# Optimization experiments

Measured on AMD Instinct MI355X. Metric: run time of the kernel, lower is better.

Reference implementation:

```python
import jax, jax.numpy as jnp
import numpy as np

B, N, D, H, O = 4096, 128, 64, 256, 128  # batch, memory_size, memory_dim, controller_dim, output_size


def setup_inputs() -> dict:
    key = jax.random.key(0)
    ks = jax.random.split(key, 20)
    s = 0.05
    inp = {
        "x": jax.random.normal(ks[0], (B, O), jnp.float32),
        "memory": jax.random.normal(ks[1], (B, N, D), jnp.float32),
        "h": jax.random.normal(ks[2], (B, H), jnp.float32),
        "c": jax.random.normal(ks[3], (B, H), jnp.float32),
        # LSTMCell params (torch layout: gates ordered i, f, g, o; input = x||read_vec of width O+D)
        "W_ih": jax.random.normal(ks[4], (4 * H, O + D), jnp.float32) * s,
        "W_hh": jax.random.normal(ks[5], (4 * H, H), jnp.float32) * s,
        "b_ih": jax.random.normal(ks[6], (4 * H,), jnp.float32) * s,
        "b_hh": jax.random.normal(ks[7], (4 * H,), jnp.float32) * s,
        "W_read": jax.random.normal(ks[8], (N, H), jnp.float32) * s,
        "b_read": jax.random.normal(ks[9], (N,), jnp.float32) * s,
        "W_write": jax.random.normal(ks[10], (N, H), jnp.float32) * s,
        "b_write": jax.random.normal(ks[11], (N,), jnp.float32) * s,
        "W_erase": jax.random.normal(ks[12], (D, H), jnp.float32) * s,
        "b_erase": jax.random.normal(ks[13], (D,), jnp.float32) * s,
        "W_add": jax.random.normal(ks[14], (D, H), jnp.float32) * s,
        "b_add": jax.random.normal(ks[15], (D,), jnp.float32) * s,
        "W_out": jax.random.normal(ks[16], (O, H + D), jnp.float32) * s,
        "b_out": jax.random.normal(ks[17], (O,), jnp.float32) * s,
    }
    return inp


def reference(x, memory, h, c, W_ih, W_hh, b_ih, b_hh, W_read, b_read,
              W_write, b_write, W_erase, b_erase, W_add, b_add, W_out, b_out):
    # read: softmax attention over memory rows, addressed by previous hidden state
    read_w = jax.nn.softmax(h @ W_read.T + b_read, axis=-1)          # [B, N]
    read_vec = jnp.einsum("bn,bnd->bd", read_w, memory)               # [B, D]

    # LSTMCell step (torch gate order: i, f, g, o)
    ctrl_in = jnp.concatenate([x, read_vec], axis=-1)                 # [B, O+D]
    gates = ctrl_in @ W_ih.T + b_ih + h @ W_hh.T + b_hh               # [B, 4H]
    i, f, g, o = jnp.split(gates, 4, axis=-1)
    i, f, o = jax.nn.sigmoid(i), jax.nn.sigmoid(f), jax.nn.sigmoid(o)
    g = jnp.tanh(g)
    c_new = f * c + i * g
    h_new = o * jnp.tanh(c_new)

    # write: outer-product erase/add update
    write_w = jax.nn.softmax(h_new @ W_write.T + b_write, axis=-1)    # [B, N]
    erase = jax.nn.sigmoid(h_new @ W_erase.T + b_erase)               # [B, D]
    add = jnp.tanh(h_new @ W_add.T + b_add)                           # [B, D]
    ww = write_w[:, :, None]                                          # [B, N, 1]
    mem_new = memory * (1.0 - ww * erase[:, None, :]) + ww * add[:, None, :]

    out = jnp.concatenate([h_new, read_vec], axis=-1) @ W_out.T + b_out  # [B, O]
    return (out, mem_new, h_new, c_new)
```

## Files before the change

kernel.cpp:

```cpp
#include <hip/hip_runtime.h>
#include <math.h>


typedef __attribute__((ext_vector_type(8))) short bf16x8;
typedef __attribute__((ext_vector_type(4))) float f32x4;
typedef __attribute__((ext_vector_type(4))) unsigned short us4;

#define MFMA16(a, b, c) __builtin_amdgcn_mfma_f32_16x16x32_bf16(a, b, c, 0, 0, 0)
#define GLL16(gp, lp) __builtin_amdgcn_global_load_lds( \
    (const __attribute__((address_space(1))) void*)(gp), \
    (__attribute__((address_space(3))) void*)(lp), 16, 0, 0)
#define SW(row, s) ((s) ^ ((row) & 3))

__device__ __forceinline__ float sigf(float v) { return 1.f / (1.f + __expf(-v)); }

__device__ __forceinline__ unsigned short f2bf(float f) {
    unsigned u = __builtin_bit_cast(unsigned, f);
    u = (u + 0x7FFFu + ((u >> 16) & 1u)) >> 16;
    return (unsigned short)u;
}

__device__ __forceinline__ int swA(int r, int c) {
    return r * 320 + (c & ~31) + ((((c >> 3) & 3) ^ (r & 3)) << 3) + (c & 7);
}

__global__ __launch_bounds__(256) void kA_scores(
    const float* __restrict__ h, const float* __restrict__ Wr,
    const float* __restrict__ br, float* __restrict__ read_w)
{
    __shared__ unsigned short As[16 * 32];
    __shared__ unsigned short Bs[128 * 32];
    __shared__ float sc[16][128];

    int t = threadIdx.x;
    int wid = t >> 6, lane = t & 63;
    int cl = lane & 15, ks = lane >> 4;
    int b0 = blockIdx.x * 16;

    int aOff = cl * 32 + SW(cl, ks) * 8;
    int bOff[4];
#pragma unroll
    for (int f = 0; f < 4; ++f) {
        int br_ = (wid * 4 + f) * 16 + cl;
        bOff[f] = br_ * 32 + SW(br_, ks) * 8;
    }
    f32x4 acc[4] = {};
    for (int kc = 0; kc < 8; ++kc) {
        __syncthreads();
        {
            int row = t >> 4, k0 = (t & 15) * 2;
            float2 hv = *(const float2*)(h + (size_t)(b0 + row) * 256 + kc * 32 + k0);
            unsigned pk = (unsigned)f2bf(hv.x) | ((unsigned)f2bf(hv.y) << 16);
            *(unsigned*)(As + row * 32 + SW(row, k0 >> 3) * 8 + (k0 & 7)) = pk;
        }
        {
            int row = t >> 1, k0 = (t & 1) * 16;
            const float4* wp = (const float4*)(Wr + (size_t)row * 256 + kc * 32 + k0);
            float4 w0 = wp[0], w1 = wp[1], w2 = wp[2], w3 = wp[3];
            us4 p0 = { f2bf(w0.x), f2bf(w0.y), f2bf(w0.z), f2bf(w0.w) };
            us4 p1 = { f2bf(w1.x), f2bf(w1.y), f2bf(w1.z), f2bf(w1.w) };
            us4 p2 = { f2bf(w2.x), f2bf(w2.y), f2bf(w2.z), f2bf(w2.w) };
            us4 p3 = { f2bf(w3.x), f2bf(w3.y), f2bf(w3.z), f2bf(w3.w) };
            int g0 = k0 >> 3;
            unsigned short* basep = Bs + row * 32;
            *(us4*)(basep + SW(row, g0) * 8)         = p0;
            *(us4*)(basep + SW(row, g0) * 8 + 4)     = p1;
            *(us4*)(basep + SW(row, g0 + 1) * 8)     = p2;
            *(us4*)(basep + SW(row, g0 + 1) * 8 + 4) = p3;
        }
        __syncthreads();
        if (wid < 2) {
            bf16x8 a = *(const bf16x8*)(As + aOff);
#pragma unroll
            for (int f = 0; f < 4; ++f)
                acc[f] = MFMA16(a, *(const bf16x8*)(Bs + bOff[f]), acc[f]);
        }
    }
    if (wid < 2) {
#pragma unroll
        for (int f = 0; f < 4; ++f)
#pragma unroll
            for (int r = 0; r < 4; ++r)
                sc[ks * 4 + r][(wid * 4 + f) * 16 + cl] = acc[f][r];
    }
    __syncthreads();
    {
        int row = t >> 4, l = t & 15;
        float v[8];
#pragma unroll
        for (int j = 0; j < 8; ++j) v[j] = sc[row][l + 16 * j] + br[l + 16 * j];
        float m = v[0];
#pragma unroll
        for (int j = 1; j < 8; ++j) m = fmaxf(m, v[j]);
#pragma unroll
        for (int mk = 8; mk >= 1; mk >>= 1) m = fmaxf(m, __shfl_xor(m, mk));
        float s = 0.f;
#pragma unroll
        for (int j = 0; j < 8; ++j) { v[j] = __expf(v[j] - m); s += v[j]; }
#pragma unroll
        for (int mk = 8; mk >= 1; mk >>= 1) s += __shfl_xor(s, mk);
        float inv = 1.f / s;
#pragma unroll
        for (int j = 0; j < 8; ++j)
            read_w[(size_t)(b0 + row) * 128 + l + 16 * j] = v[j] * inv;
    }
}

__global__ __launch_bounds__(256) void k2_stream_pack(
    const float* __restrict__ mem, const float* __restrict__ read_w,
    const float* __restrict__ x, const float* __restrict__ h,
    const float* __restrict__ Wih, const float* __restrict__ Whh,
    const float* __restrict__ bih, const float* __restrict__ bhh,
    const float* __restrict__ Ww, const float* __restrict__ We,
    const float* __restrict__ Wa, const float* __restrict__ bw,
    const float* __restrict__ be, const float* __restrict__ ba,
    const float* __restrict__ Wo,
    unsigned short* __restrict__ Wg, unsigned short* __restrict__ Wh_b,
    unsigned short* __restrict__ Wo_b, float* __restrict__ bsum,
    float* __restrict__ bh_b, unsigned short* __restrict__ Ag,
    float* __restrict__ rvf)
{
    __shared__ float part[16][68];
    int t = threadIdx.x;
    int b = blockIdx.x;
    unsigned idx = b * 256 + t;

    if (idx < 458752) {
        int r = idx / 448, cc = idx - r * 448;
        float v = (cc < 192) ? Wih[(size_t)r * 192 + cc] : Whh[(size_t)r * 256 + (cc - 192)];
        Wg[idx] = f2bf(v);
    }
    if (idx < 65536) {
        int r = idx >> 8, cc = idx & 255;
        float v = (r < 128) ? Ww[(size_t)r * 256 + cc]
                : (r < 192) ? We[(size_t)(r - 128) * 256 + cc]
                            : Wa[(size_t)(r - 192) * 256 + cc];
        Wh_b[idx] = f2bf(v);
    }
    if (idx < 40960) Wo_b[idx] = f2bf(Wo[idx]);
    if (idx < 1024)  bsum[idx] = bih[idx] + bhh[idx];
    if (idx < 256)
        bh_b[idx] = (idx < 128) ? bw[idx] : (idx < 192 ? be[idx - 128] : ba[idx - 192]);

    if (t < 96) {
        int j = t;
        float4 v = (j < 32) ? ((const float4*)(x + (size_t)b * 128))[j]
                            : ((const float4*)(h + (size_t)b * 256))[j - 32];
        us4 o = { f2bf(v.x), f2bf(v.y), f2bf(v.z), f2bf(v.w) };
        int col = (j < 32) ? j * 4 : 192 + (j - 32) * 4;
        *(us4*)(Ag + (size_t)b * 448 + col) = o;
    }

    int np = t >> 4, d4 = t & 15;
    const float4* m4 = (const float4*)(mem + (size_t)b * 8192);
    float4 acc = make_float4(0.f, 0.f, 0.f, 0.f);
#pragma unroll
    for (int j = 0; j < 8; ++j) {
        int n = np + 16 * j;
        float w = read_w[(size_t)b * 128 + n];
        float4 mv = m4[t + 256 * j];
        acc.x += w * mv.x; acc.y += w * mv.y; acc.z += w * mv.z; acc.w += w * mv.w;
    }
    part[np][d4 * 4 + 0] = acc.x; part[np][d4 * 4 + 1] = acc.y;
    part[np][d4 * 4 + 2] = acc.z; part[np][d4 * 4 + 3] = acc.w;
    __syncthreads();
    if (t < 64) {
        float s = 0.f;
#pragma unroll
        for (int q = 0; q < 16; ++q) s += part[q][t];
        Ag[(size_t)b * 448 + 128 + t] = f2bf(s);
        rvf[(size_t)b * 64 + t] = s;
    }
}

__global__ __launch_bounds__(256) void kB_gates(
    const unsigned short* __restrict__ Ag, const unsigned short* __restrict__ Wg,
    const float* __restrict__ bsum, const float* __restrict__ c,
    float* __restrict__ h_new, float* __restrict__ c_new)
{
    __shared__ unsigned short As[32 * 32];
    __shared__ unsigned short Bs[256 * 32];
    int t = threadIdx.x;
    int wid = t >> 6, lane = t & 63;
    int cl = lane & 15, ks = lane >> 4;
    int b0 = blockIdx.x * 32;
    int u0 = blockIdx.y * 64;

    int arow = (t >> 2) & 31;
    const unsigned short* aSrc = Ag + (size_t)(b0 + arow) * 448 + SW(arow, t & 3) * 8;
    unsigned short* aDst = As + wid * 512;
    const unsigned short* bSrc[4];
    unsigned short* bDst[4];
#pragma unroll
    for (int j = 0; j < 4; ++j) {
        int rl = (j * 256 + t) >> 2;
        int g = rl >> 6, u = rl & 63;
        bSrc[j] = Wg + (size_t)(g * 256 + u0 + u) * 448 + SW(rl, t & 3) * 8;
        bDst[j] = Bs + (j * 256 + wid * 64) * 8;
    }

    int aOff[2];
#pragma unroll
    for (int rf = 0; rf < 2; ++rf) {
        int mr = rf * 16 + cl;
        aOff[rf] = mr * 32 + SW(mr, ks) * 8;
    }
    int bOff[4];
#pragma unroll
    for (int g = 0; g < 4; ++g) {
        int br_ = g * 64 + wid * 16 + cl;
        bOff[g] = br_ * 32 + SW(br_, ks) * 8;
    }

    f32x4 acc[2][4] = {};
    for (int kc = 0; kc < 14; ++kc) {
        __syncthreads();
        if (wid < 2) GLL16(aSrc, aDst);
        GLL16(bSrc[0], bDst[0]); GLL16(bSrc[1], bDst[1]);
        GLL16(bSrc[2], bDst[2]); GLL16(bSrc[3], bDst[3]);
        aSrc += 32;
#pragma unroll
        for (int j = 0; j < 4; ++j) bSrc[j] += 32;
        __syncthreads();
        bf16x8 a[2], b[4];
#pragma unroll
        for (int rf = 0; rf < 2; ++rf) a[rf] = *(const bf16x8*)(As + aOff[rf]);
#pragma unroll
        for (int g = 0; g < 4; ++g) b[g] = *(const bf16x8*)(Bs + bOff[g]);
#pragma unroll
        for (int rf = 0; rf < 2; ++rf)
#pragma unroll
            for (int g = 0; g < 4; ++g)
                acc[rf][g] = MFMA16(a[rf], b[g], acc[rf][g]);
    }

    int unit = u0 + wid * 16 + cl;
    float bi = bsum[unit], bf_ = bsum[256 + unit];
    float bg = bsum[512 + unit], bo_ = bsum[768 + unit];
#pragma unroll
    for (int rf = 0; rf < 2; ++rf) {
#pragma unroll
        for (int r = 0; r < 4; ++r) {
            int row = b0 + rf * 16 + ks * 4 + r;
            float iv = sigf(acc[rf][0][r] + bi);
            float fv = sigf(acc[rf][1][r] + bf_);
            float gv = tanhf(acc[rf][2][r] + bg);
            float ov = sigf(acc[rf][3][r] + bo_);
            float cv = fv * c[(size_t)row * 256 + unit] + iv * gv;
            float hv = ov * tanhf(cv);
            c_new[(size_t)row * 256 + unit] = cv;
            h_new[(size_t)row * 256 + unit] = hv;
        }
    }
}

__global__ __launch_bounds__(256) void kC5(
    const float* __restrict__ h_new, const float* __restrict__ rvf,
    const unsigned short* __restrict__ Wh_b, const unsigned short* __restrict__ Wo_b,
    const float* __restrict__ bh_b, const float* __restrict__ bo,
    const float* __restrict__ mem, float* __restrict__ outp,
    float* __restrict__ mem_new)
{
    __shared__ unsigned short As[4 * 320];
    __shared__ unsigned short Bh[256 * 32];
    __shared__ unsigned short Bo[128 * 32];
    __shared__ float sc[4][384];
    __shared__ float wL[4][128];
    __shared__ __align__(16) float eL[4][64];
    __shared__ __align__(16) float aL[4][64];

    int t = threadIdx.x;
    int wid = t >> 6, lane = t & 63;
    int cl = lane & 15, ks = lane >> 4;
    int b0 = blockIdx.x * 4;

    for (int i = t; i < 4 * 320; i += 256) {
        int row = i / 320, col = i - row * 320;
        float v = (col < 256) ? h_new[(size_t)(b0 + row) * 256 + col]
                              : rvf[(size_t)(b0 + row) * 64 + (col - 256)];
        As[swA(row, col)] = f2bf(v);
    }

    const unsigned short* bhSrc[4];
    unsigned short* bhDst[4];
#pragma unroll
    for (int j = 0; j < 4; ++j) {
        int rl = (j * 256 + t) >> 2;
        bhSrc[j] = Wh_b + (size_t)rl * 256 + SW(rl, t & 3) * 8;
        bhDst[j] = Bh + (j * 256 + wid * 64) * 8;
    }
    const unsigned short* boSrc[2];
    unsigned short* boDst[2];
#pragma unroll
    for (int j = 0; j < 2; ++j) {
        int rj = j * 64 + (t >> 2);
        boSrc[j] = Wo_b + (size_t)rj * 320 + SW(rj, t & 3) * 8;
        boDst[j] = Bo + j * 2048 + wid * 512;
    }

    int bOffH[4], bOffO[2];
#pragma unroll
    for (int j = 0; j < 4; ++j) { int br_ = (wid + 4 * j) * 16 + cl; bOffH[j] = br_ * 32 + SW(br_, ks) * 8; }
#pragma unroll
    for (int j = 0; j < 2; ++j) { int br_ = (wid + 4 * j) * 16 + cl; bOffO[j] = br_ * 32 + SW(br_, ks) * 8; }

    f32x4 accH[4] = {};
    f32x4 accO[2] = {};
    for (int kc = 0; kc < 10; ++kc) {
        __syncthreads();
        if (kc < 8) {
            GLL16(bhSrc[0], bhDst[0]); GLL16(bhSrc[1], bhDst[1]);
            GLL16(bhSrc[2], bhDst[2]); GLL16(bhSrc[3], bhDst[3]);
#pragma unroll
            for (int j = 0; j < 4; ++j) bhSrc[j] += 32;
        }
        GLL16(boSrc[0], boDst[0]); GLL16(boSrc[1], boDst[1]);
#pragma unroll
        for (int j = 0; j < 2; ++j) boSrc[j] += 32;
        __syncthreads();
        bf16x8 a = *(const bf16x8*)(As + swA(cl & 3, kc * 32 + ks * 8));
        if (kc < 8) {
#pragma unroll
            for (int j = 0; j < 4; ++j)
                accH[j] = MFMA16(a, *(const bf16x8*)(Bh + bOffH[j]), accH[j]);
        }
#pragma unroll
        for (int j = 0; j < 2; ++j)
            accO[j] = MFMA16(a, *(const bf16x8*)(Bo + bOffO[j]), accO[j]);
    }

    if (ks == 0) {
#pragma unroll
        for (int j = 0; j < 4; ++j) {
            int col = (wid + 4 * j) * 16 + cl;
            float bb = bh_b[col];
#pragma unroll
            for (int r = 0; r < 4; ++r) sc[r][col] = accH[j][r] + bb;
        }
#pragma unroll
        for (int j = 0; j < 2; ++j) {
            int ocol = (wid + 4 * j) * 16 + cl;
            float bb = bo[ocol];
#pragma unroll
            for (int r = 0; r < 4; ++r)
                outp[(size_t)(b0 + r) * 128 + ocol] = accO[j][r] + bb;
        }
    }
    __syncthreads();

    if (t < 64) {
        int row = t >> 4, l = t & 15;
        float v[8];
#pragma unroll
        for (int j = 0; j < 8; ++j) v[j] = sc[row][l + 16 * j];
        float m = v[0];
#pragma unroll
        for (int j = 1; j < 8; ++j) m = fmaxf(m, v[j]);
#pragma unroll
        for (int mk = 8; mk >= 1; mk >>= 1) m = fmaxf(m, __shfl_xor(m, mk));
        float s = 0.f;
#pragma unroll
        for (int j = 0; j < 8; ++j) { v[j] = __expf(v[j] - m); s += v[j]; }
#pragma unroll
        for (int mk = 8; mk >= 1; mk >>= 1) s += __shfl_xor(s, mk);
        float inv = 1.f / s;
#pragma unroll
        for (int j = 0; j < 8; ++j) wL[row][l + 16 * j] = v[j] * inv;
#pragma unroll
        for (int j = 0; j < 4; ++j) eL[row][l + 16 * j] = sigf(sc[row][128 + l + 16 * j]);
#pragma unroll
        for (int j = 0; j < 4; ++j) aL[row][l + 16 * j] = tanhf(sc[row][192 + l + 16 * j]);
    }
    __syncthreads();

    {
        int r = wid;
        const f32x4* m4 = (const f32x4*)(mem + (size_t)(b0 + r) * 8192);
        f32x4* o4 = (f32x4*)(mem_new + (size_t)(b0 + r) * 8192);
        f32x4 e4 = *(const f32x4*)&eL[r][(lane & 15) * 4];
        f32x4 a4 = *(const f32x4*)&aL[r][(lane & 15) * 4];
        f32x4 one = {1.f, 1.f, 1.f, 1.f};
#pragma unroll
        for (int j = 0; j < 32; ++j) {
            int idx = j * 64 + lane;
            float w = wL[r][j * 4 + (lane >> 4)];
            f32x4 m = m4[idx];
            f32x4 res = m * (one - e4 * w) + a4 * w;
            __builtin_nontemporal_store(res, &o4[idx]);
        }
    }
}

extern "C" void kernel_launch(void* const* d_in, const int* in_sizes, int n_in,
                              void* d_out, int out_size, void* d_ws, size_t ws_size,
                              hipStream_t stream)
{
    const float* x    = (const float*)d_in[0];
    const float* mem  = (const float*)d_in[1];
    const float* h    = (const float*)d_in[2];
    const float* c    = (const float*)d_in[3];
    const float* Wih  = (const float*)d_in[4];
    const float* Whh  = (const float*)d_in[5];
    const float* bih  = (const float*)d_in[6];
    const float* bhh  = (const float*)d_in[7];
    const float* Wr   = (const float*)d_in[8];
    const float* br   = (const float*)d_in[9];
    const float* Ww   = (const float*)d_in[10];
    const float* bw   = (const float*)d_in[11];
    const float* We   = (const float*)d_in[12];
    const float* be   = (const float*)d_in[13];
    const float* Wa   = (const float*)d_in[14];
    const float* ba   = (const float*)d_in[15];
    const float* Wo   = (const float*)d_in[16];
    const float* bo   = (const float*)d_in[17];

    float* out     = (float*)d_out;
    float* mem_new = out + 524288;
    float* h_new   = out + 34078720;
    float* c_new   = out + 35127296;

    float* ws      = (float*)d_ws;
    float* read_w  = ws;
    float* bsum    = ws + 524288;
    float* bh_b    = ws + 525312;
    float* rvf     = ws + 525568;
    unsigned short* ub   = (unsigned short*)(ws + 787712);
    unsigned short* Ag   = ub;
    unsigned short* Wg   = ub + 1835008;
    unsigned short* Wh_b = ub + 2293760;
    unsigned short* Wo_b = ub + 2359296;

    kA_scores<<<256, 256, 0, stream>>>(h, Wr, br, read_w);
    k2_stream_pack<<<4096, 256, 0, stream>>>(mem, read_w, x, h, Wih, Whh, bih, bhh,
                                             Ww, We, Wa, bw, be, ba, Wo,
                                             Wg, Wh_b, Wo_b, bsum, bh_b, Ag, rvf);
    kB_gates<<<dim3(128, 4), 256, 0, stream>>>(Ag, Wg, bsum, c, h_new, c_new);
    kC5<<<1024, 256, 0, stream>>>(h_new, rvf, Wh_b, Wo_b, bh_b, bo, mem, out, mem_new);
}
```

Before: 109.2 us.

## Fuse read-score softmax into streaming pack kernel and emit bf16 activations directly

Merges the read-attention score kernel into the memory-streaming/pack kernel, so read weights are computed in fp32 FMA from shared memory and never round-trip through global memory. That removes one launch and the read_w buffer. kB_gates now writes bf16 h_new into a packed Aout buffer that the final kernel loads directly instead of converting fp32 h_new and rvf. The final kernel processes 8 batch rows per block instead of 4, using two MFMA row groups. In exchange, the score GEMM moves from MFMA to scalar FMA, and each kS block now redundantly reloads the whole W_read matrix.

```diff
diff --git a/kernel.cpp b/kernel.cpp
--- a/kernel.cpp
+++ b/kernel.cpp
@@ -20,97 +20,16 @@
     return (unsigned short)u;
 }
 
-__device__ __forceinline__ int swA(int r, int c) {
+__device__ __forceinline__ int swA8(int r, int c) {
     return r * 320 + (c & ~31) + ((((c >> 3) & 3) ^ (r & 3)) << 3) + (c & 7);
 }
 
-__global__ __launch_bounds__(256) void kA_scores(
-    const float* __restrict__ h, const float* __restrict__ Wr,
-    const float* __restrict__ br, float* __restrict__ read_w)
-{
-    __shared__ unsigned short As[16 * 32];
-    __shared__ unsigned short Bs[128 * 32];
-    __shared__ float sc[16][128];
-
-    int t = threadIdx.x;
-    int wid = t >> 6, lane = t & 63;
-    int cl = lane & 15, ks = lane >> 4;
-    int b0 = blockIdx.x * 16;
-
-    int aOff = cl * 32 + SW(cl, ks) * 8;
-    int bOff[4];
-#pragma unroll
-    for (int f = 0; f < 4; ++f) {
-        int br_ = (wid * 4 + f) * 16 + cl;
-        bOff[f] = br_ * 32 + SW(br_, ks) * 8;
-    }
-    f32x4 acc[4] = {};
-    for (int kc = 0; kc < 8; ++kc) {
-        __syncthreads();
-        {
-            int row = t >> 4, k0 = (t & 15) * 2;
-            float2 hv = *(const float2*)(h + (size_t)(b0 + row) * 256 + kc * 32 + k0);
-            unsigned pk = (unsigned)f2bf(hv.x) | ((unsigned)f2bf(hv.y) << 16);
-            *(unsigned*)(As + row * 32 + SW(row, k0 >> 3) * 8 + (k0 & 7)) = pk;
-        }
-        {
-            int row = t >> 1, k0 = (t & 1) * 16;
-            const float4* wp = (const float4*)(Wr + (size_t)row * 256 + kc * 32 + k0);
-            float4 w0 = wp[0], w1 = wp[1], w2 = wp[2], w3 = wp[3];
-            us4 p0 = { f2bf(w0.x), f2bf(w0.y), f2bf(w0.z), f2bf(w0.w) };
-            us4 p1 = { f2bf(w1.x), f2bf(w1.y), f2bf(w1.z), f2bf(w1.w) };
-            us4 p2 = { f2bf(w2.x), f2bf(w2.y), f2bf(w2.z), f2bf(w2.w) };
-            us4 p3 = { f2bf(w3.x), f2bf(w3.y), f2bf(w3.z), f2bf(w3.w) };
-            int g0 = k0 >> 3;
-            unsigned short* basep = Bs + row * 32;
-            *(us4*)(basep + SW(row, g0) * 8)         = p0;
-            *(us4*)(basep + SW(row, g0) * 8 + 4)     = p1;
-            *(us4*)(basep + SW(row, g0 + 1) * 8)     = p2;
-            *(us4*)(basep + SW(row, g0 + 1) * 8 + 4) = p3;
-        }
-        __syncthreads();
-        if (wid < 2) {
-            bf16x8 a = *(const bf16x8*)(As + aOff);
-#pragma unroll
-            for (int f = 0; f < 4; ++f)
-                acc[f] = MFMA16(a, *(const bf16x8*)(Bs + bOff[f]), acc[f]);
-        }
-    }
-    if (wid < 2) {
-#pragma unroll
-        for (int f = 0; f < 4; ++f)
-#pragma unroll
-            for (int r = 0; r < 4; ++r)
-                sc[ks * 4 + r][(wid * 4 + f) * 16 + cl] = acc[f][r];
-    }
-    __syncthreads();
-    {
-        int row = t >> 4, l = t & 15;
-        float v[8];
-#pragma unroll
-        for (int j = 0; j < 8; ++j) v[j] = sc[row][l + 16 * j] + br[l + 16 * j];
-        float m = v[0];
-#pragma unroll
-        for (int j = 1; j < 8; ++j) m = fmaxf(m, v[j]);
-#pragma unroll
-        for (int mk = 8; mk >= 1; mk >>= 1) m = fmaxf(m, __shfl_xor(m, mk));
-        float s = 0.f;
-#pragma unroll
-        for (int j = 0; j < 8; ++j) { v[j] = __expf(v[j] - m); s += v[j]; }
-#pragma unroll
-        for (int mk = 8; mk >= 1; mk >>= 1) s += __shfl_xor(s, mk);
-        float inv = 1.f / s;
-#pragma unroll
-        for (int j = 0; j < 8; ++j)
-            read_w[(size_t)(b0 + row) * 128 + l + 16 * j] = v[j] * inv;
-    }
-}
-
-__global__ __launch_bounds__(256) void k2_stream_pack(
-    const float* __restrict__ mem, const float* __restrict__ read_w,
+__global__ __launch_bounds__(256) void kS(
     const float* __restrict__ x, const float* __restrict__ h,
+    const float* __restrict__ mem,
     const float* __restrict__ Wih, const float* __restrict__ Whh,
     const float* __restrict__ bih, const float* __restrict__ bhh,
+    const float* __restrict__ Wr, const float* __restrict__ br,
     const float* __restrict__ Ww, const float* __restrict__ We,
     const float* __restrict__ Wa, const float* __restrict__ bw,
     const float* __restrict__ be, const float* __restrict__ ba,
@@ -118,65 +37,133 @@
     unsigned short* __restrict__ Wg, unsigned short* __restrict__ Wh_b,
     unsigned short* __restrict__ Wo_b, float* __restrict__ bsum,
     float* __restrict__ bh_b, unsigned short* __restrict__ Ag,
-    float* __restrict__ rvf)
+    unsigned short* __restrict__ Aout)
 {
-    __shared__ float part[16][68];
+    __shared__ float hT[8][264];
+    __shared__ float Ws[128][33];
+    __shared__ float scr[8][128];
+    __shared__ float wL[8][128];
+
     int t = threadIdx.x;
-    int b = blockIdx.x;
-    unsigned idx = b * 256 + t;
-
-    if (idx < 458752) {
-        int r = idx / 448, cc = idx - r * 448;
+    int bid = blockIdx.x;
+    int r0 = bid * 8;
+    unsigned idx = bid * 256 + t;
+
+    for (unsigned i = idx; i < 458752u; i += 131072u) {
+        int r = i / 448, cc = i - r * 448;
         float v = (cc < 192) ? Wih[(size_t)r * 192 + cc] : Whh[(size_t)r * 256 + (cc - 192)];
-        Wg[idx] = f2bf(v);
-    }
-    if (idx < 65536) {
+        Wg[i] = f2bf(v);
+    }
+    if (idx < 65536u) {
         int r = idx >> 8, cc = idx & 255;
         float v = (r < 128) ? Ww[(size_t)r * 256 + cc]
                 : (r < 192) ? We[(size_t)(r - 128) * 256 + cc]
                             : Wa[(size_t)(r - 192) * 256 + cc];
         Wh_b[idx] = f2bf(v);
     }
-    if (idx < 40960) Wo_b[idx] = f2bf(Wo[idx]);
-    if (idx < 1024)  bsum[idx] = bih[idx] + bhh[idx];
-    if (idx < 256)
+    if (idx < 40960u) Wo_b[idx] = f2bf(Wo[idx]);
+    if (idx < 1024u)  bsum[idx] = bih[idx] + bhh[idx];
+    if (idx < 256u)
         bh_b[idx] = (idx < 128) ? bw[idx] : (idx < 192 ? be[idx - 128] : ba[idx - 192]);
 
-    if (t < 96) {
-        int j = t;
-        float4 v = (j < 32) ? ((const float4*)(x + (size_t)b * 128))[j]
-                            : ((const float4*)(h + (size_t)b * 256))[j - 32];
+    {
+        int row = t >> 5, j = t & 31;
+        float4 v = ((const float4*)(x + (size_t)(r0 + row) * 128))[j];
         us4 o = { f2bf(v.x), f2bf(v.y), f2bf(v.z), f2bf(v.w) };
-        int col = (j < 32) ? j * 4 : 192 + (j - 32) * 4;
-        *(us4*)(Ag + (size_t)b * 448 + col) = o;
-    }
-
-    int np = t >> 4, d4 = t & 15;
-    const float4* m4 = (const float4*)(mem + (size_t)b * 8192);
-    float4 acc = make_float4(0.f, 0.f, 0.f, 0.f);
-#pragma unroll
-    for (int j = 0; j < 8; ++j) {
-        int n = np + 16 * j;
-        float w = read_w[(size_t)b * 128 + n];
-        float4 mv = m4[t + 256 * j];
-        acc.x += w * mv.x; acc.y += w * mv.y; acc.z += w * mv.z; acc.w += w * mv.w;
-    }
-    part[np][d4 * 4 + 0] = acc.x; part[np][d4 * 4 + 1] = acc.y;
-    part[np][d4 * 4 + 2] = acc.z; part[np][d4 * 4 + 3] = acc.w;
+        *(us4*)(Ag + (size_t)(r0 + row) * 448 + j * 4) = o;
+    }
+    for (int i = t; i < 512; i += 256) {
+        int row = i >> 6, j = i & 63;
+        float4 v = ((const float4*)(h + (size_t)(r0 + row) * 256))[j];
+        us4 o = { f2bf(v.x), f2bf(v.y), f2bf(v.z), f2bf(v.w) };
+        *(us4*)(Ag + (size_t)(r0 + row) * 448 + 192 + j * 4) = o;
+        hT[row][j * 4 + 0] = v.x; hT[row][j * 4 + 1] = v.y;
+        hT[row][j * 4 + 2] = v.z; hT[row][j * 4 + 3] = v.w;
+    }
+
+    int col = t & 127, rp = t >> 7;
+    float a0 = 0.f, a1 = 0.f, a2 = 0.f, a3 = 0.f;
+    for (int ch = 0; ch < 8; ++ch) {
+        __syncthreads();
+        for (int i = t; i < 1024; i += 256) {
+            int wr = i >> 3, j = i & 7;
+            float4 v = ((const float4*)(Wr + (size_t)wr * 256 + ch * 32))[j];
+            Ws[wr][j * 4 + 0] = v.x; Ws[wr][j * 4 + 1] = v.y;
+            Ws[wr][j * 4 + 2] = v.z; Ws[wr][j * 4 + 3] = v.w;
+        }
+        __syncthreads();
+#pragma unroll
+        for (int k = 0; k < 32; ++k) {
+            float wv = Ws[col][k];
+            int kk = ch * 32 + k;
+            a0 += hT[rp * 4 + 0][kk] * wv;
+            a1 += hT[rp * 4 + 1][kk] * wv;
+            a2 += hT[rp * 4 + 2][kk] * wv;
+            a3 += hT[rp * 4 + 3][kk] * wv;
+        }
+    }
+    {
+        float bb = br[col];
+        scr[rp * 4 + 0][col] = a0 + bb;
+        scr[rp * 4 + 1][col] = a1 + bb;
+        scr[rp * 4 + 2][col] = a2 + bb;
+        scr[rp * 4 + 3][col] = a3 + bb;
+    }
     __syncthreads();
-    if (t < 64) {
+
+    if (t < 128) {
+        int row = t >> 4, l = t & 15;
+        float v[8];
+#pragma unroll
+        for (int j = 0; j < 8; ++j) v[j] = scr[row][l + 16 * j];
+        float m = v[0];
+#pragma unroll
+        for (int j = 1; j < 8; ++j) m = fmaxf(m, v[j]);
+#pragma unroll
+        for (int mk = 8; mk >= 1; mk >>= 1) m = fmaxf(m, __shfl_xor(m, mk));
         float s = 0.f;
 #pragma unroll
-        for (int q = 0; q < 16; ++q) s += part[q][t];
-        Ag[(size_t)b * 448 + 128 + t] = f2bf(s);
-        rvf[(size_t)b * 64 + t] = s;
+        for (int j = 0; j < 8; ++j) { v[j] = __expf(v[j] - m); s += v[j]; }
+#pragma unroll
+        for (int mk = 8; mk >= 1; mk >>= 1) s += __shfl_xor(s, mk);
+        float inv = 1.f / s;
+#pragma unroll
+        for (int j = 0; j < 8; ++j) wL[row][l + 16 * j] = v[j] * inv;
+    }
+    __syncthreads();
+
+    {
+        int w = t >> 6, lane = t & 63;
+        int dg = lane & 15, ng = lane >> 4;
+#pragma unroll
+        for (int rr = 0; rr < 2; ++rr) {
+            int r = w * 2 + rr;
+            const f32x4* m4 = (const f32x4*)(mem + (size_t)(r0 + r) * 8192);
+            f32x4 a = { 0.f, 0.f, 0.f, 0.f };
+#pragma unroll
+            for (int j = 0; j < 32; ++j) {
+                int n = ng + 4 * j;
+                a += wL[r][n] * m4[n * 16 + dg];
+            }
+#pragma unroll
+            for (int i = 0; i < 4; ++i) {
+                a[i] += __shfl_xor(a[i], 16);
+                a[i] += __shfl_xor(a[i], 32);
+            }
+            if (lane < 16) {
+                us4 o = { f2bf(a[0]), f2bf(a[1]), f2bf(a[2]), f2bf(a[3]) };
+                *(us4*)(Ag + (size_t)(r0 + r) * 448 + 128 + dg * 4) = o;
+                *(us4*)(Aout + (size_t)(r0 + r) * 320 + 256 + dg * 4) = o;
+            }
+        }
     }
 }
 
 __global__ __launch_bounds__(256) void kB_gates(
     const unsigned short* __restrict__ Ag, const unsigned short* __restrict__ Wg,
     const float* __restrict__ bsum, const float* __restrict__ c,
-    float* __restrict__ h_new, float* __restrict__ c_new)
+    float* __restrict__ h_new, float* __restrict__ c_new,
+    unsigned short* __restrict__ Aout)
 {
     __shared__ unsigned short As[32 * 32];
     __shared__ unsigned short Bs[256 * 32];
@@ -250,35 +237,34 @@
             float hv = ov * tanhf(cv);
             c_new[(size_t)row * 256 + unit] = cv;
             h_new[(size_t)row * 256 + unit] = hv;
-        }
-    }
-}
-
-__global__ __launch_bounds__(256) void kC5(
-    const float* __restrict__ h_new, const float* __restrict__ rvf,
-    const unsigned short* __restrict__ Wh_b, const unsigned short* __restrict__ Wo_b,
-    const float* __restrict__ bh_b, const float* __restrict__ bo,
-    const float* __restrict__ mem, float* __restrict__ outp,
-    float* __restrict__ mem_new)
+            Aout[(size_t)row * 320 + unit] = f2bf(hv);
+        }
+    }
+}
+
+__global__ __launch_bounds__(256) void kCH(
+    const unsigned short* __restrict__ Aout, const unsigned short* __restrict__ Wh_b,
+    const unsigned short* __restrict__ Wo_b, const float* __restrict__ bh_b,
+    const float* __restrict__ bo, const float* __restrict__ mem,
+    float* __restrict__ outp, float* __restrict__ mem_new)
 {
-    __shared__ unsigned short As[4 * 320];
+    __shared__ unsigned short As8[8 * 320];
     __shared__ unsigned short Bh[256 * 32];
     __shared__ unsigned short Bo[128 * 32];
-    __shared__ float sc[4][384];
-    __shared__ float wL[4][128];
-    __shared__ __align__(16) float eL[4][64];
-    __shared__ __align__(16) float aL[4][64];
+    __shared__ float sc8[8][256];
+    __shared__ float wL[8][128];
+    __shared__ __align__(16) float eL[8][64];
+    __shared__ __align__(16) float aL[8][64];
 
     int t = threadIdx.x;
     int wid = t >> 6, lane = t & 63;
     int cl = lane & 15, ks = lane >> 4;
-    int b0 = blockIdx.x * 4;
-
-    for (int i = t; i < 4 * 320; i += 256) {
-        int row = i / 320, col = i - row * 320;
-        float v = (col < 256) ? h_new[(size_t)(b0 + row) * 256 + col]
-                              : rvf[(size_t)(b0 + row) * 64 + (col - 256)];
-        As[swA(row, col)] = f2bf(v);
+    int r0 = blockIdx.x * 8;
+
+    for (int i = t; i < 640; i += 256) {
+        int row = i / 80, c4 = (i - row * 80) * 4;
+        us4 v = *(const us4*)(Aout + (size_t)(r0 + row) * 320 + c4);
+        *(us4*)(As8 + swA8(row, c4)) = v;
     }
 
     const unsigned short* bhSrc[4];
@@ -318,7 +304,7 @@
 #pragma unroll
         for (int j = 0; j < 2; ++j) boSrc[j] += 32;
         __syncthreads();
-        bf16x8 a = *(const bf16x8*)(As + swA(cl & 3, kc * 32 + ks * 8));
+        bf16x8 a = *(const bf16x8*)(As8 + swA8(cl & 7, kc * 32 + ks * 8));
         if (kc < 8) {
 #pragma unroll
             for (int j = 0; j < 4; ++j)
@@ -329,13 +315,13 @@
             accO[j] = MFMA16(a, *(const bf16x8*)(Bo + bOffO[j]), accO[j]);
     }
 
-    if (ks == 0) {
+    if (ks < 2) {
 #pragma unroll
         for (int j = 0; j < 4; ++j) {
             int col = (wid + 4 * j) * 16 + cl;
             float bb = bh_b[col];
 #pragma unroll
-            for (int r = 0; r < 4; ++r) sc[r][col] = accH[j][r] + bb;
+            for (int r = 0; r < 4; ++r) sc8[ks * 4 + r][col] = accH[j][r] + bb;
         }
 #pragma unroll
         for (int j = 0; j < 2; ++j) {
@@ -343,16 +329,16 @@
             float bb = bo[ocol];
 #pragma unroll
             for (int r = 0; r < 4; ++r)
-                outp[(size_t)(b0 + r) * 128 + ocol] = accO[j][r] + bb;
+                outp[(size_t)(r0 + ks * 4 + r) * 128 + ocol] = accO[j][r] + bb;
         }
     }
     __syncthreads();
 
-    if (t < 64) {
+    if (t < 128) {
         int row = t >> 4, l = t & 15;
         float v[8];
 #pragma unroll
-        for (int j = 0; j < 8; ++j) v[j] = sc[row][l + 16 * j];
+        for (int j = 0; j < 8; ++j) v[j] = sc8[row][l + 16 * j];
         float m = v[0];
 #pragma unroll
         for (int j = 1; j < 8; ++j) m = fmaxf(m, v[j]);
@@ -367,26 +353,29 @@
 #pragma unroll
         for (int j = 0; j < 8; ++j) wL[row][l + 16 * j] = v[j] * inv;
 #pragma unroll
-        for (int j = 0; j < 4; ++j) eL[row][l + 16 * j] = sigf(sc[row][128 + l + 16 * j]);
-#pragma unroll
-        for (int j = 0; j < 4; ++j) aL[row][l + 16 * j] = tanhf(sc[row][192 + l + 16 * j]);
+        for (int j = 0; j < 4; ++j) eL[row][l + 16 * j] = sigf(sc8[row][128 + l + 16 * j]);
+#pragma unroll
+        for (int j = 0; j < 4; ++j) aL[row][l + 16 * j] = tanhf(sc8[row][192 + l + 16 * j]);
     }
     __syncthreads();
 
     {
-        int r = wid;
-        const f32x4* m4 = (const f32x4*)(mem + (size_t)(b0 + r) * 8192);
-        f32x4* o4 = (f32x4*)(mem_new + (size_t)(b0 + r) * 8192);
-        f32x4 e4 = *(const f32x4*)&eL[r][(lane & 15) * 4];
-        f32x4 a4 = *(const f32x4*)&aL[r][(lane & 15) * 4];
-        f32x4 one = {1.f, 1.f, 1.f, 1.f};
-#pragma unroll
-        for (int j = 0; j < 32; ++j) {
-            int idx = j * 64 + lane;
-            float w = wL[r][j * 4 + (lane >> 4)];
-            f32x4 m = m4[idx];
-            f32x4 res = m * (one - e4 * w) + a4 * w;
-            __builtin_nontemporal_store(res, &o4[idx]);
+        f32x4 one = { 1.f, 1.f, 1.f, 1.f };
+#pragma unroll
+        for (int rr = 0; rr < 2; ++rr) {
+            int r = wid * 2 + rr;
+            const f32x4* m4 = (const f32x4*)(mem + (size_t)(r0 + r) * 8192);
+            f32x4* o4 = (f32x4*)(mem_new + (size_t)(r0 + r) * 8192);
+            f32x4 e4 = *(const f32x4*)&eL[r][(lane & 15) * 4];
+            f32x4 a4 = *(const f32x4*)&aL[r][(lane & 15) * 4];
+#pragma unroll
+            for (int j = 0; j < 32; ++j) {
+                int fi = j * 64 + lane;
+                float wv = wL[r][j * 4 + (lane >> 4)];
+                f32x4 m = m4[fi];
+                f32x4 res = m * (one - e4 * wv) + a4 * wv;
+                __builtin_nontemporal_store(res, &o4[fi]);
+            }
         }
     }
 }
@@ -419,21 +408,19 @@
     float* h_new   = out + 34078720;
     float* c_new   = out + 35127296;
 
-    float* ws      = (float*)d_ws;
-    float* read_w  = ws;
-    float* bsum    = ws + 524288;
-    float* bh_b    = ws + 525312;
-    float* rvf     = ws + 525568;
-    unsigned short* ub   = (unsigned short*)(ws + 787712);
+    float* ws   = (float*)d_ws;
+    float* bsum = ws;
+    float* bh_b = ws + 1024;
+    unsigned short* ub   = (unsigned short*)(ws + 1280);
     unsigned short* Ag   = ub;
-    unsigned short* Wg   = ub + 1835008;
-    unsigned short* Wh_b = ub + 2293760;
-    unsigned short* Wo_b = ub + 2359296;
-
-    kA_scores<<<256, 256, 0, stream>>>(h, Wr, br, read_w);
-    k2_stream_pack<<<4096, 256, 0, stream>>>(mem, read_w, x, h, Wih, Whh, bih, bhh,
-                                             Ww, We, Wa, bw, be, ba, Wo,
-                                             Wg, Wh_b, Wo_b, bsum, bh_b, Ag, rvf);
-    kB_gates<<<dim3(128, 4), 256, 0, stream>>>(Ag, Wg, bsum, c, h_new, c_new);
-    kC5<<<1024, 256, 0, stream>>>(h_new, rvf, Wh_b, Wo_b, bh_b, bo, mem, out, mem_new);
-}
+    unsigned short* Aout = ub + 1835008;
+    unsigned short* Wg   = ub + 3145728;
+    unsigned short* Wh_b = ub + 3604480;
+    unsigned short* Wo_b = ub + 3670016;
+
+    kS<<<512, 256, 0, stream>>>(x, h, mem, Wih, Whh, bih, bhh, Wr, br,
+                                Ww, We, Wa, bw, be, ba, Wo,
+                                Wg, Wh_b, Wo_b, bsum, bh_b, Ag, Aout);
+    kB_gates<<<dim3(128, 4), 256, 0, stream>>>(Ag, Wg, bsum, c, h_new, c_new, Aout);
+    kCH<<<512, 256, 0, stream>>>(Aout, Wh_b, Wo_b, bh_b, bo, mem, out, mem_new);
+}
```

Result: slower. 113.9 us (+4.3%).

## Pre-pack bf16 activations for final kernel and process eight rows per block

Applied to the files above, without the earlier changes.

The gates and read-vector kernels now also write bf16 copies of h_new and read_vec into a packed [B,320] buffer. The final kernel loads that buffer with vector loads instead of converting fp32 h_new and rvf itself. The final kernel now handles 8 batch rows per block instead of 4, so each block uses more MFMA rows per weight-tile load and the grid halves to 512 blocks. This cuts redundant weight staging per row, at the cost of fewer blocks, more LDS per block, and extra scattered bf16 writes in the gates kernel.

```diff
diff --git a/kernel.cpp b/kernel.cpp
--- a/kernel.cpp
+++ b/kernel.cpp
@@ -20,7 +20,7 @@
     return (unsigned short)u;
 }
 
-__device__ __forceinline__ int swA(int r, int c) {
+__device__ __forceinline__ int swA8(int r, int c) {
     return r * 320 + (c & ~31) + ((((c >> 3) & 3) ^ (r & 3)) << 3) + (c & 7);
 }
 
@@ -118,7 +118,7 @@
     unsigned short* __restrict__ Wg, unsigned short* __restrict__ Wh_b,
     unsigned short* __restrict__ Wo_b, float* __restrict__ bsum,
     float* __restrict__ bh_b, unsigned short* __restrict__ Ag,
-    float* __restrict__ rvf)
+    unsigned short* __restrict__ Aout)
 {
     __shared__ float part[16][68];
     int t = threadIdx.x;
@@ -168,15 +168,17 @@
         float s = 0.f;
 #pragma unroll
         for (int q = 0; q < 16; ++q) s += part[q][t];
-        Ag[(size_t)b * 448 + 128 + t] = f2bf(s);
-        rvf[(size_t)b * 64 + t] = s;
+        unsigned short bv = f2bf(s);
+        Ag[(size_t)b * 448 + 128 + t] = bv;
+        Aout[(size_t)b * 320 + 256 + t] = bv;
     }
 }
 
 __global__ __launch_bounds__(256) void kB_gates(
     const unsigned short* __restrict__ Ag, const unsigned short* __restrict__ Wg,
     const float* __restrict__ bsum, const float* __restrict__ c,
-    float* __restrict__ h_new, float* __restrict__ c_new)
+    float* __restrict__ h_new, float* __restrict__ c_new,
+    unsigned short* __restrict__ Aout)
 {
     __shared__ unsigned short As[32 * 32];
     __shared__ unsigned short Bs[256 * 32];
@@ -250,35 +252,34 @@
             float hv = ov * tanhf(cv);
             c_new[(size_t)row * 256 + unit] = cv;
             h_new[(size_t)row * 256 + unit] = hv;
-        }
-    }
-}
-
-__global__ __launch_bounds__(256) void kC5(
-    const float* __restrict__ h_new, const float* __restrict__ rvf,
-    const unsigned short* __restrict__ Wh_b, const unsigned short* __restrict__ Wo_b,
-    const float* __restrict__ bh_b, const float* __restrict__ bo,
-    const float* __restrict__ mem, float* __restrict__ outp,
-    float* __restrict__ mem_new)
+            Aout[(size_t)row * 320 + unit] = f2bf(hv);
+        }
+    }
+}
+
+__global__ __launch_bounds__(256) void kCH(
+    const unsigned short* __restrict__ Aout, const unsigned short* __restrict__ Wh_b,
+    const unsigned short* __restrict__ Wo_b, const float* __restrict__ bh_b,
+    const float* __restrict__ bo, const float* __restrict__ mem,
+    float* __restrict__ outp, float* __restrict__ mem_new)
 {
-    __shared__ unsigned short As[4 * 320];
+    __shared__ unsigned short As8[8 * 320];
     __shared__ unsigned short Bh[256 * 32];
     __shared__ unsigned short Bo[128 * 32];
-    __shared__ float sc[4][384];
-    __shared__ float wL[4][128];
-    __shared__ __align__(16) float eL[4][64];
-    __shared__ __align__(16) float aL[4][64];
+    __shared__ float sc8[8][256];
+    __shared__ float wL[8][128];
+    __shared__ __align__(16) float eL[8][64];
+    __shared__ __align__(16) float aL[8][64];
 
     int t = threadIdx.x;
     int wid = t >> 6, lane = t & 63;
     int cl = lane & 15, ks = lane >> 4;
-    int b0 = blockIdx.x * 4;
-
-    for (int i = t; i < 4 * 320; i += 256) {
-        int row = i / 320, col = i - row * 320;
-        float v = (col < 256) ? h_new[(size_t)(b0 + row) * 256 + col]
-                              : rvf[(size_t)(b0 + row) * 64 + (col - 256)];
-        As[swA(row, col)] = f2bf(v);
+    int r0 = blockIdx.x * 8;
+
+    for (int i = t; i < 640; i += 256) {
+        int row = i / 80, c4 = (i - row * 80) * 4;
+        us4 v = *(const us4*)(Aout + (size_t)(r0 + row) * 320 + c4);
+        *(us4*)(As8 + swA8(row, c4)) = v;
     }
 
     const unsigned short* bhSrc[4];
@@ -318,7 +319,7 @@
 #pragma unroll
         for (int j = 0; j < 2; ++j) boSrc[j] += 32;
         __syncthreads();
-        bf16x8 a = *(const bf16x8*)(As + swA(cl & 3, kc * 32 + ks * 8));
+        bf16x8 a = *(const bf16x8*)(As8 + swA8(cl & 7, kc * 32 + ks * 8));
         if (kc < 8) {
 #pragma unroll
             for (int j = 0; j < 4; ++j)
@@ -329,13 +330,13 @@
             accO[j] = MFMA16(a, *(const bf16x8*)(Bo + bOffO[j]), accO[j]);
     }
 
-    if (ks == 0) {
+    if (ks < 2) {
 #pragma unroll
         for (int j = 0; j < 4; ++j) {
             int col = (wid + 4 * j) * 16 + cl;
             float bb = bh_b[col];
 #pragma unroll
-            for (int r = 0; r < 4; ++r) sc[r][col] = accH[j][r] + bb;
+            for (int r = 0; r < 4; ++r) sc8[ks * 4 + r][col] = accH[j][r] + bb;
         }
 #pragma unroll
         for (int j = 0; j < 2; ++j) {
@@ -343,16 +344,16 @@
             float bb = bo[ocol];
 #pragma unroll
             for (int r = 0; r < 4; ++r)
-                outp[(size_t)(b0 + r) * 128 + ocol] = accO[j][r] + bb;
+                outp[(size_t)(r0 + ks * 4 + r) * 128 + ocol] = accO[j][r] + bb;
         }
     }
     __syncthreads();
 
-    if (t < 64) {
+    if (t < 128) {
         int row = t >> 4, l = t & 15;
         float v[8];
 #pragma unroll
-        for (int j = 0; j < 8; ++j) v[j] = sc[row][l + 16 * j];
+        for (int j = 0; j < 8; ++j) v[j] = sc8[row][l + 16 * j];
         float m = v[0];
 #pragma unroll
         for (int j = 1; j < 8; ++j) m = fmaxf(m, v[j]);
@@ -367,26 +368,29 @@
 #pragma unroll
         for (int j = 0; j < 8; ++j) wL[row][l + 16 * j] = v[j] * inv;
 #pragma unroll
-        for (int j = 0; j < 4; ++j) eL[row][l + 16 * j] = sigf(sc[row][128 + l + 16 * j]);
-#pragma unroll
-        for (int j = 0; j < 4; ++j) aL[row][l + 16 * j] = tanhf(sc[row][192 + l + 16 * j]);
+        for (int j = 0; j < 4; ++j) eL[row][l + 16 * j] = sigf(sc8[row][128 + l + 16 * j]);
+#pragma unroll
+        for (int j = 0; j < 4; ++j) aL[row][l + 16 * j] = tanhf(sc8[row][192 + l + 16 * j]);
     }
     __syncthreads();
 
     {
-        int r = wid;
-        const f32x4* m4 = (const f32x4*)(mem + (size_t)(b0 + r) * 8192);
-        f32x4* o4 = (f32x4*)(mem_new + (size_t)(b0 + r) * 8192);
-        f32x4 e4 = *(const f32x4*)&eL[r][(lane & 15) * 4];
-        f32x4 a4 = *(const f32x4*)&aL[r][(lane & 15) * 4];
-        f32x4 one = {1.f, 1.f, 1.f, 1.f};
-#pragma unroll
-        for (int j = 0; j < 32; ++j) {
-            int idx = j * 64 + lane;
-            float w = wL[r][j * 4 + (lane >> 4)];
-            f32x4 m = m4[idx];
-            f32x4 res = m * (one - e4 * w) + a4 * w;
-            __builtin_nontemporal_store(res, &o4[idx]);
+        f32x4 one = { 1.f, 1.f, 1.f, 1.f };
+#pragma unroll
+        for (int rr = 0; rr < 2; ++rr) {
+            int r = wid * 2 + rr;
+            const f32x4* m4 = (const f32x4*)(mem + (size_t)(r0 + r) * 8192);
+            f32x4* o4 = (f32x4*)(mem_new + (size_t)(r0 + r) * 8192);
+            f32x4 e4 = *(const f32x4*)&eL[r][(lane & 15) * 4];
+            f32x4 a4 = *(const f32x4*)&aL[r][(lane & 15) * 4];
+#pragma unroll
+            for (int j = 0; j < 32; ++j) {
+                int fi = j * 64 + lane;
+                float wv = wL[r][j * 4 + (lane >> 4)];
+                f32x4 m = m4[fi];
+                f32x4 res = m * (one - e4 * wv) + a4 * wv;
+                __builtin_nontemporal_store(res, &o4[fi]);
+            }
         }
     }
 }
@@ -423,17 +427,17 @@
     float* read_w  = ws;
     float* bsum    = ws + 524288;
     float* bh_b    = ws + 525312;
-    float* rvf     = ws + 525568;
-    unsigned short* ub   = (unsigned short*)(ws + 787712);
+    unsigned short* ub   = (unsigned short*)(ws + 525568);
     unsigned short* Ag   = ub;
-    unsigned short* Wg   = ub + 1835008;
-    unsigned short* Wh_b = ub + 2293760;
-    unsigned short* Wo_b = ub + 2359296;
+    unsigned short* Aout = ub + 1835008;
+    unsigned short* Wg   = ub + 3145728;
+    unsigned short* Wh_b = ub + 3604480;
+    unsigned short* Wo_b = ub + 3670016;
 
     kA_scores<<<256, 256, 0, stream>>>(h, Wr, br, read_w);
     k2_stream_pack<<<4096, 256, 0, stream>>>(mem, read_w, x, h, Wih, Whh, bih, bhh,
                                              Ww, We, Wa, bw, be, ba, Wo,
-                                             Wg, Wh_b, Wo_b, bsum, bh_b, Ag, rvf);
-    kB_gates<<<dim3(128, 4), 256, 0, stream>>>(Ag, Wg, bsum, c, h_new, c_new);
-    kC5<<<1024, 256, 0, stream>>>(h_new, rvf, Wh_b, Wo_b, bh_b, bo, mem, out, mem_new);
-}
+                                             Wg, Wh_b, Wo_b, bsum, bh_b, Ag, Aout);
+    kB_gates<<<dim3(128, 4), 256, 0, stream>>>(Ag, Wg, bsum, c, h_new, c_new, Aout);
+    kCH<<<512, 256, 0, stream>>>(Aout, Wh_b, Wo_b, bh_b, bo, mem, out, mem_new);
+}
```

After: 105.1 us. -3.7%, faster.
